# Kernel tuning notes

Measured on AMD Instinct MI355X. Metric: run time of the kernel, lower is better.

The kernel has to match this reference:

```python
import jax, jax.numpy as jnp
import numpy as np

BLOCK = 32  # GGML quantization block size (Q4_0 style)
Q_OFFSET = 8.0  # 4-bit values stored unsigned in [0,16), centered by -8


def setup_inputs() -> dict:
    key = jax.random.key(0)
    k1, k2, k3, k4, k5, k6 = jax.random.split(key, 6)
    O, I, R, T = 4096, 4096, 16, 8192
    x = jax.random.normal(k1, (T, I), dtype=jnp.float32)
    qweight = jax.random.randint(k2, (O, I), 0, 16, dtype=jnp.int32)
    scales = jax.random.uniform(k3, (O, I // BLOCK), dtype=jnp.float32)
    lora_a = jax.random.normal(k4, (O, R), dtype=jnp.float32)
    lora_b = jax.random.normal(k5, (R, I), dtype=jnp.float32)
    bias = jax.random.normal(k6, (O,), dtype=jnp.float32)
    return {"x": x, "qweight": qweight, "scales": scales,
            "lora_a": lora_a, "lora_b": lora_b, "bias": bias}


def reference(x, qweight, scales, lora_a, lora_b, bias):
    # --- dequantize_tensor: per-block scale * centered int codes ---
    O, I = qweight.shape
    q = qweight.astype(jnp.float32) - Q_OFFSET            # [O, I]
    w = (q.reshape(O, I // BLOCK, BLOCK) * scales[:, :, None]).reshape(O, I)
    # --- patch application (LoRA-style additive patch) ---
    w = w + lora_a @ lora_b                               # [O, I]
    # --- downstream consumption: linear layer ---
    y = x @ w.T + bias                                    # [T, O]
    return y
```

## Files before the change

### kernel.cpp

```cpp
#include <hip/hip_runtime.h>
#include <hip/hip_bf16.h>

typedef unsigned short u16;
typedef __attribute__((ext_vector_type(16))) float f32x16;
typedef __attribute__((ext_vector_type(8))) short bf16x8;
typedef __attribute__((ext_vector_type(8))) u16 u16x8;

#define GLDS16(g, l) __builtin_amdgcn_global_load_lds( \
    (const __attribute__((address_space(1))) void*)(g), \
    (__attribute__((address_space(3))) void*)(l), 16, 0, 0)

__device__ inline u16 f2bf(float f) {
  union { float f; unsigned u; } v; v.f = f;
  unsigned r = v.u + 0x7fffu + ((v.u >> 16) & 1u);
  return (u16)(r >> 16);
}

__global__ __launch_bounds__(256) void k_dequant_lora(
    const int* __restrict__ qw, const float* __restrict__ sc,
    const float* __restrict__ la, const float* __restrict__ lb,
    u16* __restrict__ W)
{
  const int I = 4096, R = 16;
  __shared__ float lbs[16][512];
  __shared__ float las[256];
  const int c0 = blockIdx.x * 512;
  const int o0 = blockIdx.y * 16;
  const int tid = threadIdx.x;

  las[tid] = la[(size_t)(o0 + (tid >> 4)) * R + (tid & 15)];
  #pragma unroll
  for (int i = 0; i < 8; ++i) {
    int idx = tid + i * 256;
    int r = idx >> 7;
    int cc4 = (idx & 127) << 2;
    *(float4*)&lbs[r][cc4] = *(const float4*)&lb[(size_t)r * I + c0 + cc4];
  }
  __syncthreads();

  const int cc = (tid & 63) * 8;
  const int rg = tid >> 6;
  #pragma unroll
  for (int rr = 0; rr < 4; ++rr) {
    const int o = o0 + rg * 4 + rr;
    float acc[8] = {0.f,0.f,0.f,0.f,0.f,0.f,0.f,0.f};
    #pragma unroll
    for (int r = 0; r < 16; ++r) {
      float av = las[(rg * 4 + rr) * 16 + r];
      float4 b0 = *(const float4*)&lbs[r][cc];
      float4 b1 = *(const float4*)&lbs[r][cc + 4];
      acc[0] += av * b0.x; acc[1] += av * b0.y;
      acc[2] += av * b0.z; acc[3] += av * b0.w;
      acc[4] += av * b1.x; acc[5] += av * b1.y;
      acc[6] += av * b1.z; acc[7] += av * b1.w;
    }
    const int4* qp = (const int4*)&qw[(size_t)o * I + c0 + cc];
    int4 q0 = qp[0], q1 = qp[1];
    float s = sc[(size_t)o * (I / 32) + ((c0 + cc) >> 5)];
    u16x8 w;
    w[0] = f2bf(((float)q0.x - 8.0f) * s + acc[0]);
    w[1] = f2bf(((float)q0.y - 8.0f) * s + acc[1]);
    w[2] = f2bf(((float)q0.z - 8.0f) * s + acc[2]);
    w[3] = f2bf(((float)q0.w - 8.0f) * s + acc[3]);
    w[4] = f2bf(((float)q1.x - 8.0f) * s + acc[4]);
    w[5] = f2bf(((float)q1.y - 8.0f) * s + acc[5]);
    w[6] = f2bf(((float)q1.z - 8.0f) * s + acc[6]);
    w[7] = f2bf(((float)q1.w - 8.0f) * s + acc[7]);
    *(u16x8*)&W[(size_t)o * I + c0 + cc] = w;
  }
}

__global__ __launch_bounds__(256) void k_cvt(const float* __restrict__ x,
                                             u16* __restrict__ xb)
{
  const size_t n = (size_t)8192 * 4096;
  const size_t stride = (size_t)gridDim.x * 256 * 8;
  for (size_t i = ((size_t)blockIdx.x * 256 + threadIdx.x) * 8; i < n; i += stride) {
    float4 a = *(const float4*)&x[i];
    float4 b = *(const float4*)&x[i + 4];
    u16x8 o;
    o[0] = f2bf(a.x); o[1] = f2bf(a.y); o[2] = f2bf(a.z); o[3] = f2bf(a.w);
    o[4] = f2bf(b.x); o[5] = f2bf(b.y); o[6] = f2bf(b.z); o[7] = f2bf(b.w);
    *(u16x8*)&xb[i] = o;
  }
}

__global__ __launch_bounds__(512, 1) void k_gemm(
    const u16* __restrict__ A, const u16* __restrict__ B,
    const float* __restrict__ bias, float* __restrict__ C)
{
  const int N = 4096, K = 4096;
  const int NTK = 128;
  __shared__ u16 As[4 * 8192];
  __shared__ u16 Bs[4 * 8192];

  const int bid = blockIdx.x;
  const int swz = (bid & 7) * 64 + (bid >> 3);
  const int m0 = (swz >> 4) * 256;
  const int n0 = (swz & 15) * 256;

  const int tid = threadIdx.x;
  const int wid = tid >> 6, lane = tid & 63;
  const int wid_m = wid >> 2, wid_n = wid & 3;

  const int st0 = wid;
  const int st1 = 8 + wid;
  const int srow = lane >> 2;
  const int schunk = (((lane & 3) ^ (((lane >> 5) & 1) << 1))) * 8;
  const u16* Asrc0 = A + (size_t)(m0 + st0 * 16 + srow) * K + schunk;
  const u16* Asrc1 = A + (size_t)(m0 + st1 * 16 + srow) * K + schunk;
  const u16* Bsrc0 = B + (size_t)(n0 + st0 * 16 + srow) * K + schunk;
  const u16* Bsrc1 = B + (size_t)(n0 + st1 * 16 + srow) * K + schunk;

#define STAGE_A(buf, t) do { \
    GLDS16(Asrc0 + (size_t)(t) * 32, &As[(buf) * 8192 + st0 * 512]); \
    GLDS16(Asrc1 + (size_t)(t) * 32, &As[(buf) * 8192 + st1 * 512]); } while (0)
#define STAGE_B(buf, t) do { \
    GLDS16(Bsrc0 + (size_t)(t) * 32, &Bs[(buf) * 8192 + st0 * 512]); \
    GLDS16(Bsrc1 + (size_t)(t) * 32, &Bs[(buf) * 8192 + st1 * 512]); } while (0)

  const int LA = ((lane >> 4) & 1) * 512 + (lane & 15) * 32 +
                 (((lane >> 5) * 8) ^ ((lane & 8) ? 16 : 0));
  const int wmb = wid_m * 8;
  const int wnb = wid_n * 4;

  f32x16 acc[4][2] = {};
  bf16x8 aC[4], aN[4], bA[4], bB[4];

  STAGE_A(0, 0); STAGE_B(0, 0);
  STAGE_A(1, 1); STAGE_B(1, 1);
  asm volatile("s_waitcnt vmcnt(4)" ::: "memory");
  __builtin_amdgcn_s_barrier();
  __builtin_amdgcn_sched_barrier(0);
  #pragma unroll
  for (int mi = 0; mi < 2; ++mi)
    #pragma unroll
    for (int ks = 0; ks < 2; ++ks)
      aC[mi * 2 + ks] = *(const bf16x8*)&As[(wmb + mi * 2) * 512 + (LA ^ (ks << 4))];
  #pragma unroll
  for (int ni = 0; ni < 2; ++ni)
    #pragma unroll
    for (int ks = 0; ks < 2; ++ks)
      bA[ni * 2 + ks] = *(const bf16x8*)&Bs[(wnb + ni * 2) * 512 + (LA ^ (ks << 4))];

#define TILE(T, BCUR, BNXT) do { \
    const int b_ = (T) & 3; \
    const int bn_ = ((T) + 1) & 3; \
    _Pragma("unroll") \
    for (int mi = 0; mi < 2; ++mi) { \
      _Pragma("unroll") \
      for (int ks = 0; ks < 2; ++ks) \
        aN[mi * 2 + ks] = *(const bf16x8*)&As[b_ * 8192 + (wmb + 4 + mi * 2) * 512 + (LA ^ (ks << 4))]; \
    } \
    if ((T) + 2 < NTK) STAGE_A(((T) + 2) & 3, (T) + 2); \
    __builtin_amdgcn_s_setprio(1); \
    _Pragma("unroll") \
    for (int ks = 0; ks < 2; ++ks) { \
      _Pragma("unroll") \
      for (int mi = 0; mi < 2; ++mi) { \
        _Pragma("unroll") \
        for (int ni = 0; ni < 2; ++ni) \
          acc[mi][ni] = __builtin_amdgcn_mfma_f32_32x32x16_bf16(aC[mi * 2 + ks], BCUR[ni * 2 + ks], acc[mi][ni], 0, 0, 0); \
      } \
    } \
    __builtin_amdgcn_s_setprio(0); \
    if ((T) + 2 < NTK) { \
      STAGE_B(((T) + 2) & 3, (T) + 2); \
      asm volatile("s_waitcnt vmcnt(4)" ::: "memory"); \
    } else { \
      asm volatile("s_waitcnt vmcnt(0)" ::: "memory"); \
    } \
    __builtin_amdgcn_sched_barrier(0); \
    __builtin_amdgcn_s_barrier(); \
    __builtin_amdgcn_sched_barrier(0); \
    if ((T) + 1 < NTK) { \
      _Pragma("unroll") \
      for (int mi = 0; mi < 2; ++mi) { \
        _Pragma("unroll") \
        for (int ks = 0; ks < 2; ++ks) \
          aC[mi * 2 + ks] = *(const bf16x8*)&As[bn_ * 8192 + (wmb + mi * 2) * 512 + (LA ^ (ks << 4))]; \
      } \
      _Pragma("unroll") \
      for (int ni = 0; ni < 2; ++ni) { \
        _Pragma("unroll") \
        for (int ks = 0; ks < 2; ++ks) \
          BNXT[ni * 2 + ks] = *(const bf16x8*)&Bs[bn_ * 8192 + (wnb + ni * 2) * 512 + (LA ^ (ks << 4))]; \
      } \
    } \
    __builtin_amdgcn_s_setprio(1); \
    _Pragma("unroll") \
    for (int ks = 0; ks < 2; ++ks) { \
      _Pragma("unroll") \
      for (int mi = 0; mi < 2; ++mi) { \
        _Pragma("unroll") \
        for (int ni = 0; ni < 2; ++ni) \
          acc[2 + mi][ni] = __builtin_amdgcn_mfma_f32_32x32x16_bf16(aN[mi * 2 + ks], BCUR[ni * 2 + ks], acc[2 + mi][ni], 0, 0, 0); \
      } \
    } \
    __builtin_amdgcn_s_setprio(0); \
  } while (0)

  for (int t = 0; t < NTK; t += 2) {
    TILE(t, bA, bB);
    TILE(t + 1, bB, bA);
  }
#undef TILE
#undef STAGE_A
#undef STAGE_B

  const int crow0 = m0 + wid_m * 128 + ((lane >> 5) << 2);
  const int ccol = n0 + wid_n * 64 + (lane & 31);
  #pragma unroll
  for (int ni = 0; ni < 2; ++ni) {
    float bv = bias[ccol + ni * 32];
    #pragma unroll
    for (int mi = 0; mi < 4; ++mi) {
      #pragma unroll
      for (int reg = 0; reg < 16; ++reg) {
        int row = crow0 + mi * 32 + (reg & 3) + ((reg >> 2) << 3);
        C[(size_t)row * N + ccol + ni * 32] = acc[mi][ni][reg] + bv;
      }
    }
  }
}

extern "C" void kernel_launch(void* const* d_in, const int* in_sizes, int n_in,
                              void* d_out, int out_size, void* d_ws, size_t ws_size,
                              hipStream_t stream) {
  const float* x    = (const float*)d_in[0];
  const int*   qw   = (const int*)d_in[1];
  const float* sc   = (const float*)d_in[2];
  const float* la   = (const float*)d_in[3];
  const float* lb   = (const float*)d_in[4];
  const float* bias = (const float*)d_in[5];
  float* y = (float*)d_out;

  u16* W  = (u16*)d_ws;
  u16* Xb = (u16*)((char*)d_ws + (size_t)32 * 1024 * 1024);

  dim3 gridD(4096 / 512, 4096 / 16);
  k_dequant_lora<<<gridD, 256, 0, stream>>>(qw, sc, la, lb, W);
  k_cvt<<<2048, 256, 0, stream>>>(x, Xb);
  const int ngemm = (8192 / 256) * (4096 / 256);
  k_gemm<<<ngemm, 512, 0, stream>>>(Xb, W, bias, y);
}
```

Measured before the change: 382.8 us.

## Merge dequant and x conversion into one launch; change LDS swizzle

```diff
diff --git a/kernel.cpp b/kernel.cpp
--- a/kernel.cpp
+++ b/kernel.cpp
@@ -16,72 +16,73 @@
   return (u16)(r >> 16);
 }
 
-__global__ __launch_bounds__(256) void k_dequant_lora(
+__global__ __launch_bounds__(256) void k_prep(
     const int* __restrict__ qw, const float* __restrict__ sc,
     const float* __restrict__ la, const float* __restrict__ lb,
-    u16* __restrict__ W)
+    const float* __restrict__ x,
+    u16* __restrict__ W, u16* __restrict__ xb)
 {
   const int I = 4096, R = 16;
-  __shared__ float lbs[16][512];
-  __shared__ float las[256];
-  const int c0 = blockIdx.x * 512;
-  const int o0 = blockIdx.y * 16;
   const int tid = threadIdx.x;
-
-  las[tid] = la[(size_t)(o0 + (tid >> 4)) * R + (tid & 15)];
-  #pragma unroll
-  for (int i = 0; i < 8; ++i) {
-    int idx = tid + i * 256;
-    int r = idx >> 7;
-    int cc4 = (idx & 127) << 2;
-    *(float4*)&lbs[r][cc4] = *(const float4*)&lb[(size_t)r * I + c0 + cc4];
-  }
-  __syncthreads();
-
-  const int cc = (tid & 63) * 8;
-  const int rg = tid >> 6;
-  #pragma unroll
-  for (int rr = 0; rr < 4; ++rr) {
-    const int o = o0 + rg * 4 + rr;
-    float acc[8] = {0.f,0.f,0.f,0.f,0.f,0.f,0.f,0.f};
-    #pragma unroll
-    for (int r = 0; r < 16; ++r) {
-      float av = las[(rg * 4 + rr) * 16 + r];
-      float4 b0 = *(const float4*)&lbs[r][cc];
-      float4 b1 = *(const float4*)&lbs[r][cc + 4];
-      acc[0] += av * b0.x; acc[1] += av * b0.y;
-      acc[2] += av * b0.z; acc[3] += av * b0.w;
-      acc[4] += av * b1.x; acc[5] += av * b1.y;
-      acc[6] += av * b1.z; acc[7] += av * b1.w;
-    }
-    const int4* qp = (const int4*)&qw[(size_t)o * I + c0 + cc];
-    int4 q0 = qp[0], q1 = qp[1];
-    float s = sc[(size_t)o * (I / 32) + ((c0 + cc) >> 5)];
-    u16x8 w;
-    w[0] = f2bf(((float)q0.x - 8.0f) * s + acc[0]);
-    w[1] = f2bf(((float)q0.y - 8.0f) * s + acc[1]);
-    w[2] = f2bf(((float)q0.z - 8.0f) * s + acc[2]);
-    w[3] = f2bf(((float)q0.w - 8.0f) * s + acc[3]);
-    w[4] = f2bf(((float)q1.x - 8.0f) * s + acc[4]);
-    w[5] = f2bf(((float)q1.y - 8.0f) * s + acc[5]);
-    w[6] = f2bf(((float)q1.z - 8.0f) * s + acc[6]);
-    w[7] = f2bf(((float)q1.w - 8.0f) * s + acc[7]);
-    *(u16x8*)&W[(size_t)o * I + c0 + cc] = w;
-  }
-}
-
-__global__ __launch_bounds__(256) void k_cvt(const float* __restrict__ x,
-                                             u16* __restrict__ xb)
-{
-  const size_t n = (size_t)8192 * 4096;
-  const size_t stride = (size_t)gridDim.x * 256 * 8;
-  for (size_t i = ((size_t)blockIdx.x * 256 + threadIdx.x) * 8; i < n; i += stride) {
-    float4 a = *(const float4*)&x[i];
-    float4 b = *(const float4*)&x[i + 4];
-    u16x8 o;
-    o[0] = f2bf(a.x); o[1] = f2bf(a.y); o[2] = f2bf(a.z); o[3] = f2bf(a.w);
-    o[4] = f2bf(b.x); o[5] = f2bf(b.y); o[6] = f2bf(b.z); o[7] = f2bf(b.w);
-    *(u16x8*)&xb[i] = o;
+  const int b = blockIdx.x;
+
+  if (b < 2048) {
+    __shared__ float lbs[16][512];
+    __shared__ float las[256];
+    const int c0 = (b & 7) * 512;
+    const int o0 = (b >> 3) * 16;
+
+    las[tid] = la[(size_t)(o0 + (tid >> 4)) * R + (tid & 15)];
+    #pragma unroll
+    for (int i = 0; i < 8; ++i) {
+      int idx = tid + i * 256;
+      int r = idx >> 7;
+      int cc4 = (idx & 127) << 2;
+      *(float4*)&lbs[r][cc4] = *(const float4*)&lb[(size_t)r * I + c0 + cc4];
+    }
+    __syncthreads();
+
+    const int cc = (tid & 63) * 8;
+    const int rg = tid >> 6;
+    #pragma unroll
+    for (int rr = 0; rr < 4; ++rr) {
+      const int o = o0 + rg * 4 + rr;
+      float acc[8] = {0.f,0.f,0.f,0.f,0.f,0.f,0.f,0.f};
+      #pragma unroll
+      for (int r = 0; r < 16; ++r) {
+        float av = las[(rg * 4 + rr) * 16 + r];
+        float4 b0 = *(const float4*)&lbs[r][cc];
+        float4 b1 = *(const float4*)&lbs[r][cc + 4];
+        acc[0] += av * b0.x; acc[1] += av * b0.y;
+        acc[2] += av * b0.z; acc[3] += av * b0.w;
+        acc[4] += av * b1.x; acc[5] += av * b1.y;
+        acc[6] += av * b1.z; acc[7] += av * b1.w;
+      }
+      const int4* qp = (const int4*)&qw[(size_t)o * I + c0 + cc];
+      int4 q0 = qp[0], q1 = qp[1];
+      float s = sc[(size_t)o * (I / 32) + ((c0 + cc) >> 5)];
+      u16x8 w;
+      w[0] = f2bf(((float)q0.x - 8.0f) * s + acc[0]);
+      w[1] = f2bf(((float)q0.y - 8.0f) * s + acc[1]);
+      w[2] = f2bf(((float)q0.z - 8.0f) * s + acc[2]);
+      w[3] = f2bf(((float)q0.w - 8.0f) * s + acc[3]);
+      w[4] = f2bf(((float)q1.x - 8.0f) * s + acc[4]);
+      w[5] = f2bf(((float)q1.y - 8.0f) * s + acc[5]);
+      w[6] = f2bf(((float)q1.z - 8.0f) * s + acc[6]);
+      w[7] = f2bf(((float)q1.w - 8.0f) * s + acc[7]);
+      *(u16x8*)&W[(size_t)o * I + c0 + cc] = w;
+    }
+  } else {
+    const size_t n = (size_t)8192 * 4096;
+    const size_t stride = (size_t)2048 * 256 * 8;
+    for (size_t i = ((size_t)(b - 2048) * 256 + tid) * 8; i < n; i += stride) {
+      float4 a = *(const float4*)&x[i];
+      float4 c = *(const float4*)&x[i + 4];
+      u16x8 o;
+      o[0] = f2bf(a.x); o[1] = f2bf(a.y); o[2] = f2bf(a.z); o[3] = f2bf(a.w);
+      o[4] = f2bf(c.x); o[5] = f2bf(c.y); o[6] = f2bf(c.z); o[7] = f2bf(c.w);
+      *(u16x8*)&xb[i] = o;
+    }
   }
 }
 
@@ -106,7 +107,7 @@
   const int st0 = wid;
   const int st1 = 8 + wid;
   const int srow = lane >> 2;
-  const int schunk = (((lane & 3) ^ (((lane >> 5) & 1) << 1))) * 8;
+  const int schunk = ((lane & 3) ^ ((lane >> 3) & 3)) * 8;
   const u16* Asrc0 = A + (size_t)(m0 + st0 * 16 + srow) * K + schunk;
   const u16* Asrc1 = A + (size_t)(m0 + st1 * 16 + srow) * K + schunk;
   const u16* Bsrc0 = B + (size_t)(n0 + st0 * 16 + srow) * K + schunk;
@@ -120,7 +121,7 @@
     GLDS16(Bsrc1 + (size_t)(t) * 32, &Bs[(buf) * 8192 + st1 * 512]); } while (0)
 
   const int LA = ((lane >> 4) & 1) * 512 + (lane & 15) * 32 +
-                 (((lane >> 5) * 8) ^ ((lane & 8) ? 16 : 0));
+                 (((lane >> 5) ^ ((lane >> 1) & 3)) * 8);
   const int wmb = wid_m * 8;
   const int wnb = wid_n * 4;
 
@@ -238,9 +239,7 @@
   u16* W  = (u16*)d_ws;
   u16* Xb = (u16*)((char*)d_ws + (size_t)32 * 1024 * 1024);
 
-  dim3 gridD(4096 / 512, 4096 / 16);
-  k_dequant_lora<<<gridD, 256, 0, stream>>>(qw, sc, la, lb, W);
-  k_cvt<<<2048, 256, 0, stream>>>(x, Xb);
+  k_prep<<<4096, 256, 0, stream>>>(qw, sc, la, lb, x, W, Xb);
   const int ngemm = (8192 / 256) * (4096 / 256);
   k_gemm<<<ngemm, 512, 0, stream>>>(Xb, W, bias, y);
 }
```

Measured after the change: 397.4 us. 1.04x slower.
